# Optimization experiments

Hardware: AMD Instinct MI355X
Metric: run time of the kernel (lower is better)

## Reference

```python
import jax, jax.numpy as jnp
import numpy as np

HEADS = 4
KNN_K = 20
BN_EPS = 1e-5


def conv1x1(w, b, x):
    # 1x1 Conv1d: w [out, in], x [B, in, N] -> [B, out, N]
    return jnp.einsum('oc,bcn->bon', w, x) + b[None, :, None]


def setup_inputs() -> dict:
    key = jax.random.key(0)
    B, C, N = 2, 128, 2048
    ks = jax.random.split(key, 16)
    W = lambda k, o, i: jax.random.normal(k, (o, i), jnp.float32) * 0.05
    V = lambda k, o: jax.random.normal(k, (o,), jnp.float32) * 0.05
    return {
        'desc1': jax.random.normal(ks[0], (B, C, N, 1), jnp.float32),
        'wq': W(ks[1], C, C), 'bq': V(ks[2], C),
        'wk': W(ks[3], C, C), 'bk': V(ks[4], C),
        'wv': W(ks[5], C, C), 'bv': V(ks[6], C),
        'wm': W(ks[7], C, C), 'bm': V(ks[8], C),
        'w1': W(ks[9], 2 * C, 2 * C), 'b1': V(ks[10], 2 * C),
        'gamma': jnp.ones((2 * C,), jnp.float32),
        'beta': jnp.zeros((2 * C,), jnp.float32),
        'w2': W(ks[11], C, 2 * C), 'b2': V(ks[12], C),
    }


def reference(desc1, wq, bq, wk, bk, wv, bv, wm, bm, w1, b1, gamma, beta, w2, b2):
    x = desc1[..., 0]                      # [B, C, N]
    B, C, N = x.shape
    D = C // HEADS

    q = conv1x1(wq, bq, x).reshape(B, HEADS, D, N)
    k = conv1x1(wk, bk, x).reshape(B, HEADS, D, N)
    v = conv1x1(wv, bv, x).reshape(B, HEADS, D, N)

    # kNN on raw descriptors: pd = -||xi||^2 + 2 xi.xj - ||xj||^2 (larger = closer)
    xx = jnp.sum(x * x, axis=1)            # [B, N]
    pd = 2.0 * jnp.einsum('bcn,bcm->bnm', x, x) - xx[:, :, None] - xx[:, None, :]
    idx = jax.lax.top_k(pd, KNN_K)[1]      # [B, N, K]

    # scatter ones at kNN indices, then keep only mutual neighbors
    bI = jnp.arange(B)[:, None, None]
    nI = jnp.arange(N)[None, :, None]
    mask = jnp.zeros((B, N, N), x.dtype).at[bI, nI, idx].set(1.0)
    mask = mask * mask.transpose(0, 2, 1)  # [B, N, N]

    score = jnp.einsum('bhdn,bhdm->bhnm', q, k) / (D ** 0.5)
    m = mask[:, None]                      # broadcast over heads
    score = score * m + (-1e9) * (1.0 - m)
    score = jax.nn.softmax(score, axis=-1)

    av = jnp.einsum('bhnm,bhdm->bhdn', score, v).reshape(B, C, N)
    av = conv1x1(wm, bm, av)

    h = conv1x1(w1, b1, jnp.concatenate([x, av], axis=1))  # [B, 2C, N]
    mu = jnp.mean(h, axis=(0, 2), keepdims=True)
    var = jnp.var(h, axis=(0, 2), keepdims=True)           # biased, matches torch BN
    h = (h - mu) / jnp.sqrt(var + BN_EPS) * gamma[None, :, None] + beta[None, :, None]
    h = jax.nn.relu(h)

    out = x + conv1x1(w2, b2, h)
    return out[..., None]                  # [B, C, N, 1]
```

## Files before the change

### kernel.cpp

```cpp
#include <hip/hip_runtime.h>
#include <math.h>

#define NPT 2048
#define KNN 20

typedef const float* fp;
typedef __attribute__((ext_vector_type(4))) float f32x4;
typedef __attribute__((ext_vector_type(8))) short s16x8;

__device__ __forceinline__ ushort f2bf_rne(float v) {
    unsigned u = __float_as_uint(v);
    unsigned r = u + 0x7FFFu + ((u >> 16) & 1u);
    return (ushort)(r >> 16);
}
__device__ __forceinline__ float bfbits2f(ushort h) {
    return __uint_as_float(((unsigned)h) << 16);
}
__device__ __forceinline__ s16x8 ldfrag(const ushort* p) {
    union { uint4 u; s16x8 s; } cv;
    cv.u = *reinterpret_cast<const uint4*>(p);
    return cv.s;
}
__device__ __forceinline__ void f8_hilo(const float* row, s16x8* hi, s16x8* lo) {
    float4 f0 = *reinterpret_cast<const float4*>(row);
    float4 f1 = *reinterpret_cast<const float4*>(row + 4);
    float f[8] = {f0.x, f0.y, f0.z, f0.w, f1.x, f1.y, f1.z, f1.w};
    union { ushort u[8]; s16x8 s; } H, L;
    #pragma unroll
    for (int j = 0; j < 8; j++) {
        ushort h = f2bf_rne(f[j]);
        H.u[j] = h;
        L.u[j] = f2bf_rne(f[j] - bfbits2f(h));
    }
    *hi = H.s; *lo = L.s;
}

__global__ __launch_bounds__(256) void prep_all(
    fp xbf, fp wq, fp wk, fp wv, fp wm, fp w1, fp w2, fp bm, fp b1,
    float* xx, ushort* xhiF, ushort* xloF,
    ushort* wqFhi, ushort* wqFlo, ushort* wkFhi, ushort* wkFlo,
    ushort* wvFhi, ushort* wvFlo,
    ushort* wcFhi, ushort* wcFlo, ushort* w2Fhi, ushort* w2Flo,
    float* b1p, float* stats) {
    int t = threadIdx.x;
    if (blockIdx.x < 256) {
        __shared__ float xs[16][129];
        __shared__ float xpart[16][17];
        int p0 = blockIdx.x * 16;
        int b = p0 >> 11, n0 = p0 & 2047;
        fp xb = xbf + (size_t)b * 128 * NPT;
        {
            int c = t >> 1, half = t & 1;
            float4 f0 = *reinterpret_cast<const float4*>(xb + (size_t)c * NPT + n0 + half * 8);
            float4 f1 = *reinterpret_cast<const float4*>(xb + (size_t)c * NPT + n0 + half * 8 + 4);
            xs[half * 8 + 0][c] = f0.x; xs[half * 8 + 1][c] = f0.y;
            xs[half * 8 + 2][c] = f0.z; xs[half * 8 + 3][c] = f0.w;
            xs[half * 8 + 4][c] = f1.x; xs[half * 8 + 5][c] = f1.y;
            xs[half * 8 + 6][c] = f1.z; xs[half * 8 + 7][c] = f1.w;
        }
        __syncthreads();
        int p = t & 15, g = t >> 4, c0 = g * 8;
        float f[8];
        #pragma unroll
        for (int j = 0; j < 8; j++) f[j] = xs[p][c0 + j];
        float ps = 0.f;
        #pragma unroll
        for (int j = 0; j < 8; j++) ps += f[j] * f[j];
        xpart[p][g] = ps;
        union { ushort u[8]; uint4 q; } H, L;
        #pragma unroll
        for (int j = 0; j < 8; j++) {
            ushort hi = f2bf_rne(f[j]);
            H.u[j] = hi;
            L.u[j] = f2bf_rne(f[j] - bfbits2f(hi));
        }
        size_t off = ((size_t)blockIdx.x * 4 + (c0 >> 5)) * 512
                   + (size_t)(((((c0 >> 3) & 3) * 16) + p) * 8);
        *reinterpret_cast<uint4*>(xhiF + off) = H.q;
        *reinterpret_cast<uint4*>(xloF + off) = L.q;
        __syncthreads();
        if (t < 16) {
            float s = 0.f;
            #pragma unroll
            for (int gg = 0; gg < 16; gg++) s += xpart[t][gg];
            xx[p0 + t] = s;
        }
        return;
    }
    int wid = (blockIdx.x - 256) * 256 + t;
    if (wid < 49152) {
        int which = wid >> 14, e = wid & 16383;
        int lane = (e >> 3) & 63, j = e & 7, kk = (e >> 9) & 3, nt = e >> 11;
        int n = nt * 16 + (lane & 15);
        int k = kk * 32 + (lane >> 4) * 8 + j;
        fp src = which == 0 ? wq : which == 1 ? wk : wv;
        float v = src[n * 128 + k];
        ushort hi = f2bf_rne(v);
        (which == 0 ? wqFhi : which == 1 ? wkFhi : wvFhi)[e] = hi;
        (which == 0 ? wqFlo : which == 1 ? wkFlo : wvFlo)[e] = f2bf_rne(v - bfbits2f(hi));
    } else if (wid < 114688) {
        int e = wid - 49152;
        int j = e & 7, lane = (e >> 3) & 63, kk = (e >> 9) & 7, nt = e >> 12;
        int n = nt * 16 + (lane & 15);
        int k = kk * 32 + (lane >> 4) * 8 + j;
        float v;
        if (k < 128) {
            v = w1[n * 256 + k];
        } else {
            int c = k - 128;
            float s = 0.f;
            for (int i = 0; i < 128; i += 4) {
                float4 wr = *reinterpret_cast<const float4*>(w1 + n * 256 + 128 + i);
                s += wr.x * wm[(i + 0) * 128 + c];
                s += wr.y * wm[(i + 1) * 128 + c];
                s += wr.z * wm[(i + 2) * 128 + c];
                s += wr.w * wm[(i + 3) * 128 + c];
            }
            v = s;
        }
        ushort hi = f2bf_rne(v);
        wcFhi[e] = hi;
        wcFlo[e] = f2bf_rne(v - bfbits2f(hi));
    } else if (wid < 147456) {
        int e = wid - 114688;
        int j = e & 7, lane = (e >> 3) & 63, kk = (e >> 9) & 7, nt = e >> 12;
        int n = nt * 16 + (lane & 15);
        int k = kk * 32 + (lane >> 4) * 8 + j;
        float v = w2[n * 256 + k];
        ushort hi = f2bf_rne(v);
        w2Fhi[e] = hi;
        w2Flo[e] = f2bf_rne(v - bfbits2f(hi));
    } else if (wid < 147712) {
        int o = wid - 147456;
        float s = b1[o];
        for (int i = 0; i < 128; i++)
            s += w1[o * 256 + 128 + i] * bm[i];
        b1p[o] = s;
    } else {
        stats[wid - 147712] = 0.0f;
    }
}

#define MERGE(off) { float ov = __shfl_xor(bv, off); int oi = __shfl_xor(bi, off); \
                     if (ov > bv || (ov == bv && oi < bi)) { bv = ov; bi = oi; } }

#define KEYPAIR(C0, D0, D1) { \
    int ct0 = slab * 128 + w * 8 + C0; \
    int ct1 = ct0 + 1; \
    f32x4 a0 = (f32x4){0.f, 0.f, 0.f, 0.f}; \
    f32x4 a1 = (f32x4){0.f, 0.f, 0.f, 0.f}; \
    _Pragma("unroll 2") \
    for (int kk = 0; kk < 4; kk++) { \
        s16x8 ah = ldfrag(Ahi[kk] + lane * 8); \
        s16x8 al = ldfrag(Alo[kk] + lane * 8); \
        s16x8 b0h = ldfrag(xhiF + ((size_t)(ct0 * 4 + kk)) * 512 + lane * 8); \
        s16x8 b0l = ldfrag(xloF + ((size_t)(ct0 * 4 + kk)) * 512 + lane * 8); \
        s16x8 b1h = ldfrag(xhiF + ((size_t)(ct1 * 4 + kk)) * 512 + lane * 8); \
        s16x8 b1l = ldfrag(xloF + ((size_t)(ct1 * 4 + kk)) * 512 + lane * 8); \
        a0 = __builtin_amdgcn_mfma_f32_16x16x32_bf16(ah, b0h, a0, 0, 0, 0); \
        a1 = __builtin_amdgcn_mfma_f32_16x16x32_bf16(ah, b1h, a1, 0, 0, 0); \
        a0 = __builtin_amdgcn_mfma_f32_16x16x32_bf16(al, b0h, a0, 0, 0, 0); \
        a1 = __builtin_amdgcn_mfma_f32_16x16x32_bf16(al, b1h, a1, 0, 0, 0); \
        a0 = __builtin_amdgcn_mfma_f32_16x16x32_bf16(ah, b0l, a0, 0, 0, 0); \
        a1 = __builtin_amdgcn_mfma_f32_16x16x32_bf16(ah, b1l, a1, 0, 0, 0); \
    } \
    float xx0 = xx[slab * 2048 + (w * 8 + C0) * 16 + cl]; \
    float xx1 = xx[slab * 2048 + (w * 8 + C0 + 1) * 16 + cl]; \
    a0[0] = 2.0f * a0[0] - xx0; a0[1] = 2.0f * a0[1] - xx0; \
    a0[2] = 2.0f * a0[2] - xx0; a0[3] = 2.0f * a0[3] - xx0; \
    a1[0] = 2.0f * a1[0] - xx1; a1[1] = 2.0f * a1[1] - xx1; \
    a1[2] = 2.0f * a1[2] - xx1; a1[3] = 2.0f * a1[3] - xx1; \
    D0 = a0; D1 = a1; \
}

__global__ __launch_bounds__(1024, 4) void gemm_key_topk(
    const ushort* xhiF, const ushort* xloF, const float* xx,
    const ushort* wqFhi, const ushort* wqFlo,
    const ushort* wkFhi, const ushort* wkFlo,
    const ushort* wvFhi, const ushort* wvFlo,
    fp bq, fp bk, fp bv_, float* qT, float* kT, float* vT,
    float* pvv, int* pii, int* cntb, float* scratch) {
    __shared__ ushort Ahi[4][512];
    __shared__ ushort Alo[4][512];
    __shared__ float chm[16][64];
    __shared__ float sv[16][256];
    __shared__ int   si[16][256];
    __shared__ float Trow[16];
    __shared__ int   rowcnt[16];
    __shared__ int   ovfAll;
    int tt = threadIdx.x, w = tt >> 6, lane = tt & 63;
    int rt = blockIdx.x;
    int slab = rt >> 7, rtl = rt & 127;
    int cl = lane & 15, quad = lane >> 4;

    if (tt < 16) rowcnt[tt] = 0;

    if (tt < 512) {
        int which = tt >> 8, kk = (tt >> 6) & 3, ln = tt & 63;
        const ushort* src = (which ? xloF : xhiF)
                          + ((size_t)(rt * 4 + kk)) * 512 + ln * 8;
        uint4 v = *reinterpret_cast<const uint4*>(src);
        *reinterpret_cast<uint4*>((which ? Alo[kk] : Ahi[kk]) + ln * 8) = v;
    }
    __syncthreads();

    if (w < 12) {
        f32x4 acc0 = (f32x4){0.f, 0.f, 0.f, 0.f};
        f32x4 acc1 = (f32x4){0.f, 0.f, 0.f, 0.f};
        int pair0 = w * 2, pair1 = w * 2 + 1;
        int mat0 = pair0 >> 3, nt0 = pair0 & 7;
        int mat1 = pair1 >> 3, nt1 = pair1 & 7;
        const ushort* w0hi = mat0 == 0 ? wqFhi : mat0 == 1 ? wkFhi : wvFhi;
        const ushort* w0lo = mat0 == 0 ? wqFlo : mat0 == 1 ? wkFlo : wvFlo;
        const ushort* w1hi = mat1 == 0 ? wqFhi : mat1 == 1 ? wkFhi : wvFhi;
        const ushort* w1lo = mat1 == 0 ? wqFlo : mat1 == 1 ? wkFlo : wvFlo;
        #pragma unroll 2
        for (int kk = 0; kk < 4; kk++) {
            s16x8 ah = ldfrag(Ahi[kk] + lane * 8);
            s16x8 al = ldfrag(Alo[kk] + lane * 8);
            s16x8 b0h = ldfrag(w0hi + ((size_t)(nt0 * 4 + kk)) * 512 + lane * 8);
            s16x8 b0l = ldfrag(w0lo + ((size_t)(nt0 * 4 + kk)) * 512 + lane * 8);
            s16x8 b1h = ldfrag(w1hi + ((size_t)(nt1 * 4 + kk)) * 512 + lane * 8);
            s16x8 b1l = ldfrag(w1lo + ((size_t)(nt1 * 4 + kk)) * 512 + lane * 8);
            acc0 = __builtin_amdgcn_mfma_f32_16x16x32_bf16(ah, b0h, acc0, 0, 0, 0);
            acc1 = __builtin_amdgcn_mfma_f32_16x16x32_bf16(ah, b1h, acc1, 0, 0, 0);
            acc0 = __builtin_amdgcn_mfma_f32_16x16x32_bf16(al, b0h, acc0, 0, 0, 0);
            acc1 = __builtin_amdgcn_mfma_f32_16x16x32_bf16(al, b1h, acc1, 0, 0, 0);
            acc0 = __builtin_amdgcn_mfma_f32_16x16x32_bf16(ah, b0l, acc0, 0, 0, 0);
            acc1 = __builtin_amdgcn_mfma_f32_16x16x32_bf16(ah, b1l, acc1, 0, 0, 0);
        }
        int p0 = rt * 16;
        {
            fp bias    = mat0 == 0 ? bq : mat0 == 1 ? bk : bv_;
            float* out = mat0 == 0 ? qT : mat0 == 1 ? kT : vT;
            int o = nt0 * 16 + cl;
            float bvv = bias[o];
            #pragma unroll
            for (int r = 0; r < 4; r++)
                out[(size_t)(p0 + quad * 4 + r) * 128 + o] = acc0[r] + bvv;
        }
        {
            fp bias    = mat1 == 0 ? bq : mat1 == 1 ? bk : bv_;
            float* out = mat1 == 0 ? qT : mat1 == 1 ? kT : vT;
            int o = nt1 * 16 + cl;
            float bvv = bias[o];
            #pragma unroll
            for (int r = 0; r < 4; r++)
                out[(size_t)(p0 + quad * 4 + r) * 128 + o] = acc1[r] + bvv;
        }
    }
    __builtin_amdgcn_sched_barrier(0);

    f32x4 key0, key1, key2, key3, key4, key5, key6, key7;
    KEYPAIR(0, key0, key1)
    __builtin_amdgcn_sched_barrier(0);
    KEYPAIR(2, key2, key3)
    __builtin_amdgcn_sched_barrier(0);
    KEYPAIR(4, key4, key5)
    __builtin_amdgcn_sched_barrier(0);
    KEYPAIR(6, key6, key7)
    __builtin_amdgcn_sched_barrier(0);

    {
        float m[4];
        #pragma unroll
        for (int r = 0; r < 4; r++) {
            float mm = fmaxf(fmaxf(fmaxf(key0[r], key1[r]), fmaxf(key2[r], key3[r])),
                             fmaxf(fmaxf(key4[r], key5[r]), fmaxf(key6[r], key7[r])));
            mm = fmaxf(mm, __shfl_xor(mm, 1));
            mm = fmaxf(mm, __shfl_xor(mm, 2));
            m[r] = mm;
        }
        if ((cl & 3) == 0) {
            #pragma unroll
            for (int r = 0; r < 4; r++)
                chm[quad * 4 + r][w * 4 + (cl >> 2)] = m[r];
        }
    }
    __syncthreads();

    {
        float bs = chm[w][lane];
        #pragma unroll
        for (int k = 2; k <= 64; k <<= 1) {
            #pragma unroll
            for (int j = k >> 1; j > 0; j >>= 1) {
                float o = __shfl_xor(bs, j);
                bool dirDesc = (lane & k) != 0;
                bool upper   = (lane & j) != 0;
                bs = (upper != dirDesc) ? fmaxf(bs, o) : fminf(bs, o);
            }
        }
        float T = __shfl(bs, 44);
        if (lane == 0) Trow[w] = T;
    }
    __syncthreads();

    #pragma unroll
    for (int r = 0; r < 4; r++) {
        int row = quad * 4 + r;
        float T = Trow[row];
        float vals[8] = {key0[r], key1[r], key2[r], key3[r],
                         key4[r], key5[r], key6[r], key7[r]};
        #pragma unroll
        for (int c = 0; c < 8; c++) {
            float v = vals[c];
            if (v >= T) {
                int pos = atomicAdd(&rowcnt[row], 1);
                if (pos < 256) {
                    sv[row][pos] = v;
                    si[row][pos] = (w * 8 + c) * 16 + cl;
                }
            }
        }
    }
    __syncthreads();
    if (tt == 0) {
        int o = 0;
        for (int i = 0; i < 16; i++) o |= (rowcnt[i] > 256) ? 1 : 0;
        ovfAll = o;
    }
    __syncthreads();
    int ovf = ovfAll;

    int S = rowcnt[w];
    int rowg = slab * 2048 + rtl * 16 + w;
    size_t sbase = (size_t)rowg * 256;
    if (S <= 256) {
        if (lane == 0) cntb[rowg] = S;
        for (int g = lane; g < S; g += 64) {
            pvv[sbase + g] = sv[w][g];
            pii[sbase + g] = si[w][g];
        }
    }

    if (ovf) {
        #pragma unroll
        for (int r = 0; r < 4; r++) {
            float vals[8] = {key0[r], key1[r], key2[r], key3[r],
                             key4[r], key5[r], key6[r], key7[r]};
            #pragma unroll
            for (int c = 0; c < 8; c++)
                scratch[((size_t)rt * 16 + quad * 4 + r) * 2048
                        + (w * 8 + c) * 16 + cl] = vals[c];
        }
        __syncthreads();
        if (rowcnt[w] > 256) {
            const float* rowp = scratch + ((size_t)rt * 16 + w) * 2048;
            float rv[32];
            #pragma unroll
            for (int j = 0; j < 32; j++) rv[j] = rowp[j * 64 + lane];
            unsigned removed = 0u;
            for (int iter = 0; iter < KNN; iter++) {
                float bv = -3.4e38f; int bi = 0;
                #pragma unroll
                for (int sl = 0; sl < 32; sl++) {
                    bool live = ((removed >> sl) & 1u) == 0u;
                    if (live && rv[sl] > bv) { bv = rv[sl]; bi = sl * 64 + lane; }
                }
                MERGE(32) MERGE(16) MERGE(8) MERGE(4) MERGE(2) MERGE(1)
                if (lane == 0) { pvv[sbase + iter] = bv; pii[sbase + iter] = bi; }
                if ((bi & 63) == lane) removed |= 1u << (bi >> 6);
            }
            if (lane == 0) cntb[rowg] = -1;
        }
    }
}

__global__ __launch_bounds__(256) void sort_topk(
    const float* pvv, const int* pii, const int* cntb, int* idxbuf) {
    int w = threadIdx.x >> 6, lane = threadIdx.x & 63;
    int row = blockIdx.x * 4 + w;
    int S = cntb[row];
    if (S < 0) S = KNN;
    const float* v0 = pvv + (size_t)row * 256;
    const int*   i0 = pii + (size_t)row * 256;
    if (S <= 64) {
        float v; int idx;
        if (lane < S) { v = v0[lane]; idx = i0[lane]; }
        else          { v = -3.4e38f; idx = 0x7FFFFFFF; }
        #pragma unroll
        for (int k = 2; k <= 64; k <<= 1) {
            #pragma unroll
            for (int j = k >> 1; j > 0; j >>= 1) {
                float ov = __shfl_xor(v, j); int oi = __shfl_xor(idx, j);
                bool dirDesc = (lane & k) != 0;
                bool upper   = (lane & j) != 0;
                bool takeMax = (upper != dirDesc);
                bool amax = (v > ov) || (v == ov && idx < oi);
                if (takeMax != amax) { v = ov; idx = oi; }
            }
        }
        if (lane >= 44) idxbuf[(size_t)row * KNN + (63 - lane)] = idx;
    } else {
        float vl[4]; int il[4];
        #pragma unroll
        for (int s = 0; s < 4; s++) {
            int g = lane + s * 64;
            bool ok = g < S;
            vl[s] = ok ? v0[g] : -3.4e38f;
            il[s] = ok ? i0[g] : 0x7FFFFFFF;
        }
        unsigned removed = 0u;
        for (int iter = 0; iter < KNN; iter++) {
            float bv = -3.4e38f; int bi = 0x7FFFFFFF;
            #pragma unroll
            for (int s = 0; s < 4; s++) {
                bool live = ((removed >> s) & 1u) == 0u;
                if (live && (vl[s] > bv || (vl[s] == bv && il[s] < bi))) {
                    bv = vl[s]; bi = il[s];
                }
            }
            MERGE(32) MERGE(16) MERGE(8) MERGE(4) MERGE(2) MERGE(1)
            if (lane == 0) idxbuf[(size_t)row * KNN + iter] = bi;
            #pragma unroll
            for (int s = 0; s < 4; s++)
                if (il[s] == bi) removed |= 1u << s;
        }
    }
}

__global__ __launch_bounds__(256) void k3_attn(
    fp qT, fp kT, fp vT, const int* idxbuf, float* avT) {
    __shared__ float sbuf[2][KNN * 4];
    __shared__ int   mlist[2][KNN];
    __shared__ int   cnt_s[2];
    int tt = threadIdx.x;
    int half = tt >> 7, t = tt & 127;
    int p = blockIdx.x * 2 + half;
    int b = p >> 11, n = p & 2047;
    int bbase = b * NPT;
    int h = t >> 5;

    if ((tt >> 6) == half * 2) {
        int lane = tt & 63;
        bool fl = false; int m = 0;
        if (lane < KNN) {
            m = idxbuf[(size_t)p * KNN + lane] & 2047;
            const int4* mrow = reinterpret_cast<const int4*>(idxbuf + (size_t)(bbase + m) * KNN);
            int4 r0 = mrow[0], r1 = mrow[1], r2 = mrow[2], r3 = mrow[3], r4 = mrow[4];
            fl = (r0.x == n) || (r0.y == n) || (r0.z == n) || (r0.w == n)
              || (r1.x == n) || (r1.y == n) || (r1.z == n) || (r1.w == n)
              || (r2.x == n) || (r2.y == n) || (r2.z == n) || (r2.w == n)
              || (r3.x == n) || (r3.y == n) || (r3.z == n) || (r3.w == n)
              || (r4.x == n) || (r4.y == n) || (r4.z == n) || (r4.w == n);
        }
        unsigned long long mask = __ballot(fl);
        int pos = __popcll(mask & ((1ull << lane) - 1ull));
        if (fl) mlist[half][pos] = m;
        if (lane == 0) cnt_s[half] = (int)__popcll(mask);
    }
    __syncthreads();

    int cnt = cnt_s[half];
    float qv = qT[(size_t)p * 128 + t];
    for (int jj = 0; jj < cnt; jj++) {
        int m = mlist[half][jj];
        float prod = qv * kT[(size_t)(bbase + m) * 128 + t];
        prod += __shfl_xor(prod, 16);
        prod += __shfl_xor(prod, 8);
        prod += __shfl_xor(prod, 4);
        prod += __shfl_xor(prod, 2);
        prod += __shfl_xor(prod, 1);
        if ((t & 31) == 0) sbuf[half][jj * 4 + h] = prod * 0.17677669529663687f;
    }
    __syncthreads();

    float mx = -3.4e38f;
    for (int j = 0; j < cnt; j++) mx = fmaxf(mx, sbuf[half][j * 4 + h]);
    float den = 0.f;
    for (int j = 0; j < cnt; j++) den += expf(sbuf[half][j * 4 + h] - mx);
    float inv = (cnt > 0) ? (1.0f / den) : 0.0f;
    float acc = 0.f;
    for (int j = 0; j < cnt; j++) {
        float pw = expf(sbuf[half][j * 4 + h] - mx) * inv;
        acc += pw * vT[(size_t)(bbase + mlist[half][j]) * 128 + t];
    }
    avT[(size_t)p * 128 + t] = acc;
}

__global__ __launch_bounds__(1024) void k4b_h(
    const ushort* xhiF, const ushort* xloF, const float* avT,
    const ushort* wcFhi, const ushort* wcFlo,
    const float* b1p, float* hbuf, float* stats) {
    __shared__ ushort AH[8][512];
    __shared__ ushort AL[8][512];
    int tt = threadIdx.x, w = tt >> 6, lane = tt & 63;
    int rt = blockIdx.x;
    int p0 = rt * 16;

    if (w < 8) {
        int which = w & 1, kk = w >> 1;
        const ushort* src = (which ? xloF : xhiF)
                          + ((size_t)(rt * 4 + kk)) * 512 + lane * 8;
        uint4 v = *reinterpret_cast<const uint4*>(src);
        *reinterpret_cast<uint4*>((which ? AL[kk] : AH[kk]) + lane * 8) = v;
    } else if (w < 12) {
        int kk = 4 + (w - 8);
        const float* arow = avT + (size_t)(p0 + (lane & 15)) * 128
                          + (kk - 4) * 32 + (lane >> 4) * 8;
        s16x8 hi, lo;
        f8_hilo(arow, &hi, &lo);
        union { s16x8 s; uint4 u; } cvh, cvl;
        cvh.s = hi; cvl.s = lo;
        *reinterpret_cast<uint4*>(AH[kk] + lane * 8) = cvh.u;
        *reinterpret_cast<uint4*>(AL[kk] + lane * 8) = cvl.u;
    }
    __syncthreads();

    int nt = w;
    f32x4 acc = (f32x4){0.f, 0.f, 0.f, 0.f};
    for (int kk = 0; kk < 8; kk++) {
        s16x8 ahi = ldfrag(AH[kk] + lane * 8);
        s16x8 alo = ldfrag(AL[kk] + lane * 8);
        s16x8 bhi = ldfrag(wcFhi + ((size_t)(nt * 8 + kk)) * 512 + lane * 8);
        s16x8 blo = ldfrag(wcFlo + ((size_t)(nt * 8 + kk)) * 512 + lane * 8);
        acc = __builtin_amdgcn_mfma_f32_16x16x32_bf16(ahi, bhi, acc, 0, 0, 0);
        acc = __builtin_amdgcn_mfma_f32_16x16x32_bf16(alo, bhi, acc, 0, 0, 0);
        acc = __builtin_amdgcn_mfma_f32_16x16x32_bf16(ahi, blo, acc, 0, 0, 0);
    }

    int cl = lane & 15, quad = lane >> 4;
    int o = nt * 16 + cl;
    float bb = b1p[o];
    float s = 0.f, s2 = 0.f;
    #pragma unroll
    for (int r = 0; r < 4; r++) {
        float v = acc[r] + bb;
        hbuf[(size_t)(p0 + quad * 4 + r) * 256 + o] = v;
        s += v; s2 += v * v;
    }
    s  += __shfl_xor(s, 16);  s  += __shfl_xor(s, 32);
    s2 += __shfl_xor(s2, 16); s2 += __shfl_xor(s2, 32);
    if (quad == 0) {
        atomicAdd(&stats[o], s);
        atomicAdd(&stats[256 + o], s2);
    }
}

__global__ __launch_bounds__(512) void k5b_out(
    const float* hbuf, const float* stats, fp gamma, fp beta,
    const ushort* w2Fhi, const ushort* w2Flo,
    fp b2, fp xbf, float* out) {
    __shared__ ushort HH[8][512];
    __shared__ ushort HL[8][512];
    int tt = threadIdx.x, w = tt >> 6, lane = tt & 63;
    int rt = blockIdx.x;
    int p0 = rt * 16;

    {
        int kk = w;
        int c0 = kk * 32 + (lane >> 4) * 8;
        const float* hrow = hbuf + (size_t)(p0 + (lane & 15)) * 256 + c0;
        float4 f0 = *reinterpret_cast<const float4*>(hrow);
        float4 f1 = *reinterpret_cast<const float4*>(hrow + 4);
        float4 s0 = *reinterpret_cast<const float4*>(stats + c0);
        float4 s1 = *reinterpret_cast<const float4*>(stats + c0 + 4);
        float4 q0 = *reinterpret_cast<const float4*>(stats + 256 + c0);
        float4 q1 = *reinterpret_cast<const float4*>(stats + 256 + c0 + 4);
        float4 g0 = *reinterpret_cast<const float4*>(gamma + c0);
        float4 g1 = *reinterpret_cast<const float4*>(gamma + c0 + 4);
        float4 e0 = *reinterpret_cast<const float4*>(beta + c0);
        float4 e1 = *reinterpret_cast<const float4*>(beta + c0 + 4);
        float f[8] = {f0.x, f0.y, f0.z, f0.w, f1.x, f1.y, f1.z, f1.w};
        float sm[8] = {s0.x, s0.y, s0.z, s0.w, s1.x, s1.y, s1.z, s1.w};
        float sq[8] = {q0.x, q0.y, q0.z, q0.w, q1.x, q1.y, q1.z, q1.w};
        float gm[8] = {g0.x, g0.y, g0.z, g0.w, g1.x, g1.y, g1.z, g1.w};
        float bt[8] = {e0.x, e0.y, e0.z, e0.w, e1.x, e1.y, e1.z, e1.w};
        union { ushort u[8]; uint4 q; } H, L;
        #pragma unroll
        for (int j = 0; j < 8; j++) {
            float mu  = sm[j] * (1.0f / 4096.0f);
            float var = fmaxf(sq[j] * (1.0f / 4096.0f) - mu * mu, 0.0f);
            float a    = gm[j] / sqrtf(var + 1e-5f);
            float cadd = bt[j] - mu * a;
            float v = fmaxf(f[j] * a + cadd, 0.0f);
            ushort hi = f2bf_rne(v);
            H.u[j] = hi;
            L.u[j] = f2bf_rne(v - bfbits2f(hi));
        }
        *reinterpret_cast<uint4*>(HH[kk] + lane * 8) = H.q;
        *reinterpret_cast<uint4*>(HL[kk] + lane * 8) = L.q;
    }
    __syncthreads();

    int nt = w;
    f32x4 acc = (f32x4){0.f, 0.f, 0.f, 0.f};
    for (int kk = 0; kk < 8; kk++) {
        s16x8 ahi = ldfrag(HH[kk] + lane * 8);
        s16x8 alo = ldfrag(HL[kk] + lane * 8);
        s16x8 bhi = ldfrag(w2Fhi + ((size_t)(nt * 8 + kk)) * 512 + lane * 8);
        s16x8 blo = ldfrag(w2Flo + ((size_t)(nt * 8 + kk)) * 512 + lane * 8);
        acc = __builtin_amdgcn_mfma_f32_16x16x32_bf16(ahi, bhi, acc, 0, 0, 0);
        acc = __builtin_amdgcn_mfma_f32_16x16x32_bf16(alo, bhi, acc, 0, 0, 0);
        acc = __builtin_amdgcn_mfma_f32_16x16x32_bf16(ahi, blo, acc, 0, 0, 0);
    }
    int cl = lane & 15, quad = lane >> 4;
    int b = p0 >> 11, n0 = p0 & 2047;
    int o = nt * 16 + cl;
    float bb = b2[o];
    size_t base = (size_t)b * 128 * NPT + (size_t)o * NPT + n0 + quad * 4;
    float4 xv = *reinterpret_cast<const float4*>(xbf + base);
    float4 ov;
    ov.x = acc[0] + bb + xv.x;
    ov.y = acc[1] + bb + xv.y;
    ov.z = acc[2] + bb + xv.z;
    ov.w = acc[3] + bb + xv.w;
    *reinterpret_cast<float4*>(out + base) = ov;
}

#define WS_FULL 53383168u

extern "C" void kernel_launch(void* const* d_in, const int* in_sizes, int n_in,
                              void* d_out, int out_size, void* d_ws, size_t ws_size,
                              hipStream_t stream) {
    fp desc1 = (fp)d_in[0];
    fp wq = (fp)d_in[1];  fp bq = (fp)d_in[2];
    fp wk = (fp)d_in[3];  fp bk = (fp)d_in[4];
    fp wv = (fp)d_in[5];  fp bv = (fp)d_in[6];
    fp wm = (fp)d_in[7];  fp bm = (fp)d_in[8];
    fp w1 = (fp)d_in[9];  fp b1 = (fp)d_in[10];
    fp gamma = (fp)d_in[11]; fp beta = (fp)d_in[12];
    fp w2 = (fp)d_in[13]; fp b2 = (fp)d_in[14];

    if (ws_size < (size_t)WS_FULL) return;

    char* ws = (char*)d_ws;
    float*  qT    = (float*) (ws + 0);
    float*  kT    = (float*) (ws + 2097152);
    float*  vT    = (float*) (ws + 4194304);
    float*  avT   = (float*) (ws + 6291456);
    float*  xx    = (float*) (ws + 8388608);
    int*    idxb  = (int*)   (ws + 8404992);
    float*  stats = (float*) (ws + 8732672);
    float*  b1p   = (float*) (ws + 8734720);
    ushort* wqFhi = (ushort*)(ws + 8736768);
    ushort* wqFlo = (ushort*)(ws + 8769536);
    ushort* wkFhi = (ushort*)(ws + 8802304);
    ushort* wkFlo = (ushort*)(ws + 8835072);
    ushort* wvFhi = (ushort*)(ws + 8867840);
    ushort* wvFlo = (ushort*)(ws + 8900608);
    ushort* wcFhi = (ushort*)(ws + 8933376);
    ushort* wcFlo = (ushort*)(ws + 9064448);
    ushort* w2Fhi = (ushort*)(ws + 9195520);
    ushort* w2Flo = (ushort*)(ws + 9261056);
    ushort* xhiF  = (ushort*)(ws + 9326592);
    ushort* xloF  = (ushort*)(ws + 10375168);
    int*    cntb  = (int*)   (ws + 11423744);
    float*  pvv   = (float*) (ws + 11440128);
    int*    pii   = (int*)   (ws + 15634432);
    float*  scratch = (float*)(ws + 19828736);
    float*  hbuf  = (float*) (ws + 0);

    prep_all<<<835, 256, 0, stream>>>(desc1, wq, wk, wv, wm, w1, w2, bm, b1,
                                      xx, xhiF, xloF,
                                      wqFhi, wqFlo, wkFhi, wkFlo, wvFhi, wvFlo,
                                      wcFhi, wcFlo, w2Fhi, w2Flo, b1p, stats);
    gemm_key_topk<<<256, 1024, 0, stream>>>(xhiF, xloF, xx,
                                            wqFhi, wqFlo, wkFhi, wkFlo,
                                            wvFhi, wvFlo,
                                            bq, bk, bv, qT, kT, vT,
                                            pvv, pii, cntb, scratch);
    sort_topk<<<1024, 256, 0, stream>>>(pvv, pii, cntb, idxb);
    k3_attn<<<2048, 256, 0, stream>>>(qT, kT, vT, idxb, avT);
    k4b_h<<<256, 1024, 0, stream>>>(xhiF, xloF, avT, wcFhi, wcFlo,
                                    b1p, hbuf, stats);
    k5b_out<<<256, 512, 0, stream>>>(hbuf, stats, gamma, beta, w2Fhi, w2Flo,
                                     b2, desc1, (float*)d_out);
}
```

Measured before the change: 156.7 us.

## Fuse top-k sort into key GEMM kernel and single-pass softmax-AV in attention

Moves the per-row candidate sort (bitonic or iterative selection) from the separate sort_topk kernel into gemm_key_topk, reading candidates straight from shared memory and writing final indices to idxbuf. This drops one launch and the global round trip through the pvv/pii/cntb buffers, and shrinks the workspace. In k3_attn the score loop is unrolled by two, and the exp/denominator/value accumulation is merged into one pass so each exp is computed once. The risk is extra register pressure and longer tails in the large 1024-thread GEMM kernel.

```diff
diff --git a/kernel.cpp b/kernel.cpp
--- a/kernel.cpp
+++ b/kernel.cpp
@@ -179,7 +179,7 @@
     const ushort* wkFhi, const ushort* wkFlo,
     const ushort* wvFhi, const ushort* wvFlo,
     fp bq, fp bk, fp bv_, float* qT, float* kT, float* vT,
-    float* pvv, int* pii, int* cntb, float* scratch) {
+    int* idxbuf, float* scratch) {
     __shared__ ushort Ahi[4][512];
     __shared__ ushort Alo[4][512];
     __shared__ float chm[16][64];
@@ -325,12 +325,47 @@
 
     int S = rowcnt[w];
     int rowg = slab * 2048 + rtl * 16 + w;
-    size_t sbase = (size_t)rowg * 256;
-    if (S <= 256) {
-        if (lane == 0) cntb[rowg] = S;
-        for (int g = lane; g < S; g += 64) {
-            pvv[sbase + g] = sv[w][g];
-            pii[sbase + g] = si[w][g];
+    if (S <= 64) {
+        float v; int idx;
+        if (lane < S) { v = sv[w][lane]; idx = si[w][lane]; }
+        else          { v = -3.4e38f;    idx = 0x7FFFFFFF; }
+        #pragma unroll
+        for (int k = 2; k <= 64; k <<= 1) {
+            #pragma unroll
+            for (int j = k >> 1; j > 0; j >>= 1) {
+                float ov = __shfl_xor(v, j); int oi = __shfl_xor(idx, j);
+                bool dirDesc = (lane & k) != 0;
+                bool upper   = (lane & j) != 0;
+                bool takeMax = (upper != dirDesc);
+                bool amax = (v > ov) || (v == ov && idx < oi);
+                if (takeMax != amax) { v = ov; idx = oi; }
+            }
+        }
+        if (lane >= 44) idxbuf[(size_t)rowg * KNN + (63 - lane)] = idx;
+    } else if (S <= 256) {
+        float vl[4]; int il[4];
+        #pragma unroll
+        for (int s = 0; s < 4; s++) {
+            int g = lane + s * 64;
+            bool ok = g < S;
+            vl[s] = ok ? sv[w][g] : -3.4e38f;
+            il[s] = ok ? si[w][g] : 0x7FFFFFFF;
+        }
+        unsigned removed = 0u;
+        for (int iter = 0; iter < KNN; iter++) {
+            float bv = -3.4e38f; int bi = 0x7FFFFFFF;
+            #pragma unroll
+            for (int s = 0; s < 4; s++) {
+                bool live = ((removed >> s) & 1u) == 0u;
+                if (live && (vl[s] > bv || (vl[s] == bv && il[s] < bi))) {
+                    bv = vl[s]; bi = il[s];
+                }
+            }
+            MERGE(32) MERGE(16) MERGE(8) MERGE(4) MERGE(2) MERGE(1)
+            if (lane == 0) idxbuf[(size_t)rowg * KNN + iter] = bi;
+            #pragma unroll
+            for (int s = 0; s < 4; s++)
+                if (il[s] == bi) removed |= 1u << s;
         }
     }
 
@@ -359,63 +394,9 @@
                     if (live && rv[sl] > bv) { bv = rv[sl]; bi = sl * 64 + lane; }
                 }
                 MERGE(32) MERGE(16) MERGE(8) MERGE(4) MERGE(2) MERGE(1)
-                if (lane == 0) { pvv[sbase + iter] = bv; pii[sbase + iter] = bi; }
+                if (lane == 0) idxbuf[(size_t)rowg * KNN + iter] = bi;
                 if ((bi & 63) == lane) removed |= 1u << (bi >> 6);
             }
-            if (lane == 0) cntb[rowg] = -1;
-        }
-    }
-}
-
-__global__ __launch_bounds__(256) void sort_topk(
-    const float* pvv, const int* pii, const int* cntb, int* idxbuf) {
-    int w = threadIdx.x >> 6, lane = threadIdx.x & 63;
-    int row = blockIdx.x * 4 + w;
-    int S = cntb[row];
-    if (S < 0) S = KNN;
-    const float* v0 = pvv + (size_t)row * 256;
-    const int*   i0 = pii + (size_t)row * 256;
-    if (S <= 64) {
-        float v; int idx;
-        if (lane < S) { v = v0[lane]; idx = i0[lane]; }
-        else          { v = -3.4e38f; idx = 0x7FFFFFFF; }
-        #pragma unroll
-        for (int k = 2; k <= 64; k <<= 1) {
-            #pragma unroll
-            for (int j = k >> 1; j > 0; j >>= 1) {
-                float ov = __shfl_xor(v, j); int oi = __shfl_xor(idx, j);
-                bool dirDesc = (lane & k) != 0;
-                bool upper   = (lane & j) != 0;
-                bool takeMax = (upper != dirDesc);
-                bool amax = (v > ov) || (v == ov && idx < oi);
-                if (takeMax != amax) { v = ov; idx = oi; }
-            }
-        }
-        if (lane >= 44) idxbuf[(size_t)row * KNN + (63 - lane)] = idx;
-    } else {
-        float vl[4]; int il[4];
-        #pragma unroll
-        for (int s = 0; s < 4; s++) {
-            int g = lane + s * 64;
-            bool ok = g < S;
-            vl[s] = ok ? v0[g] : -3.4e38f;
-            il[s] = ok ? i0[g] : 0x7FFFFFFF;
-        }
-        unsigned removed = 0u;
-        for (int iter = 0; iter < KNN; iter++) {
-            float bv = -3.4e38f; int bi = 0x7FFFFFFF;
-            #pragma unroll
-            for (int s = 0; s < 4; s++) {
-                bool live = ((removed >> s) & 1u) == 0u;
-                if (live && (vl[s] > bv || (vl[s] == bv && il[s] < bi))) {
-                    bv = vl[s]; bi = il[s];
-                }
-            }
-            MERGE(32) MERGE(16) MERGE(8) MERGE(4) MERGE(2) MERGE(1)
-            if (lane == 0) idxbuf[(size_t)row * KNN + iter] = bi;
-            #pragma unroll
-            for (int s = 0; s < 4; s++)
-                if (il[s] == bi) removed |= 1u << s;
         }
     }
 }
@@ -454,7 +435,22 @@
 
     int cnt = cnt_s[half];
     float qv = qT[(size_t)p * 128 + t];
-    for (int jj = 0; jj < cnt; jj++) {
+    int jj = 0;
+    for (; jj + 1 < cnt; jj += 2) {
+        int m0 = mlist[half][jj], m1 = mlist[half][jj + 1];
+        float pr0 = qv * kT[(size_t)(bbase + m0) * 128 + t];
+        float pr1 = qv * kT[(size_t)(bbase + m1) * 128 + t];
+        pr0 += __shfl_xor(pr0, 16); pr1 += __shfl_xor(pr1, 16);
+        pr0 += __shfl_xor(pr0, 8);  pr1 += __shfl_xor(pr1, 8);
+        pr0 += __shfl_xor(pr0, 4);  pr1 += __shfl_xor(pr1, 4);
+        pr0 += __shfl_xor(pr0, 2);  pr1 += __shfl_xor(pr1, 2);
+        pr0 += __shfl_xor(pr0, 1);  pr1 += __shfl_xor(pr1, 1);
+        if ((t & 31) == 0) {
+            sbuf[half][jj * 4 + h]       = pr0 * 0.17677669529663687f;
+            sbuf[half][(jj + 1) * 4 + h] = pr1 * 0.17677669529663687f;
+        }
+    }
+    if (jj < cnt) {
         int m = mlist[half][jj];
         float prod = qv * kT[(size_t)(bbase + m) * 128 + t];
         prod += __shfl_xor(prod, 16);
@@ -468,15 +464,14 @@
 
     float mx = -3.4e38f;
     for (int j = 0; j < cnt; j++) mx = fmaxf(mx, sbuf[half][j * 4 + h]);
-    float den = 0.f;
-    for (int j = 0; j < cnt; j++) den += expf(sbuf[half][j * 4 + h] - mx);
+    float den = 0.f, accv = 0.f;
+    for (int j = 0; j < cnt; j++) {
+        float ex = expf(sbuf[half][j * 4 + h] - mx);
+        den += ex;
+        accv += ex * vT[(size_t)(bbase + mlist[half][j]) * 128 + t];
+    }
     float inv = (cnt > 0) ? (1.0f / den) : 0.0f;
-    float acc = 0.f;
-    for (int j = 0; j < cnt; j++) {
-        float pw = expf(sbuf[half][j * 4 + h] - mx) * inv;
-        acc += pw * vT[(size_t)(bbase + mlist[half][j]) * 128 + t];
-    }
-    avT[(size_t)p * 128 + t] = acc;
+    avT[(size_t)p * 128 + t] = accv * inv;
 }
 
 __global__ __launch_bounds__(1024) void k4b_h(
@@ -609,7 +604,7 @@
     *reinterpret_cast<float4*>(out + base) = ov;
 }
 
-#define WS_FULL 53383168u
+#define WS_FULL 44978176u
 
 extern "C" void kernel_launch(void* const* d_in, const int* in_sizes, int n_in,
                               void* d_out, int out_size, void* d_ws, size_t ws_size,
@@ -646,10 +641,7 @@
     ushort* w2Flo = (ushort*)(ws + 9261056);
     ushort* xhiF  = (ushort*)(ws + 9326592);
     ushort* xloF  = (ushort*)(ws + 10375168);
-    int*    cntb  = (int*)   (ws + 11423744);
-    float*  pvv   = (float*) (ws + 11440128);
-    int*    pii   = (int*)   (ws + 15634432);
-    float*  scratch = (float*)(ws + 19828736);
+    float*  scratch = (float*)(ws + 11423744);
     float*  hbuf  = (float*) (ws + 0);
 
     prep_all<<<835, 256, 0, stream>>>(desc1, wq, wk, wv, wm, w1, w2, bm, b1,
@@ -660,8 +652,7 @@
                                             wqFhi, wqFlo, wkFhi, wkFlo,
                                             wvFhi, wvFlo,
                                             bq, bk, bv, qT, kT, vT,
-                                            pvv, pii, cntb, scratch);
-    sort_topk<<<1024, 256, 0, stream>>>(pvv, pii, cntb, idxb);
+                                            idxb, scratch);
     k3_attn<<<2048, 256, 0, stream>>>(qT, kT, vT, idxb, avT);
     k4b_h<<<256, 1024, 0, stream>>>(xhiF, xloF, avT, wcFhi, wcFlo,
                                     b1p, hbuf, stats);
```

After: 150.5 us, median of 2. -4.0%, faster.
